# Kernel optimization log

Hardware: AMD Instinct MI355X
Metric: run time of the kernel (lower is better)

Reference implementation:

```python
import math
import jax, jax.numpy as jnp
import numpy as np

CHANNELS = 512
OUT_CHANNELS = 512
N_HEADS = 8
K_CHANNELS = CHANNELS // N_HEADS
WINDOW = 4


def _get_relative_embeddings(emb, length):
    # emb: [1, 2*WINDOW+1, d] -> [1, 2*length-1, d]
    max_rel = 2 * WINDOW + 1
    pad_length = max(0, length - (WINDOW + 1))
    start = max(0, WINDOW + 1 - length)
    end = max_rel + 2 * length - 1
    if pad_length > 0:
        emb = jnp.pad(emb, ((0, 0), (pad_length, pad_length), (0, 0)))
    return emb[:, start:end]


def _rel_to_abs(x):
    # x: [b, h, l, 2l-1] -> [b, h, l, l] via skewing trick
    b, h, l, _ = x.shape
    x = jnp.pad(x, ((0, 0), (0, 0), (0, 0), (0, 1)))
    x_flat = x.reshape(b, h, l * 2 * l)
    x_flat = jnp.pad(x_flat, ((0, 0), (0, 0), (0, l - 1)))
    return x_flat.reshape(b, h, l + 1, 2 * l - 1)[..., :l, l - 1:]


def _abs_to_rel(x):
    # x: [b, h, l, l] -> [b, h, l, 2l-1]
    b, h, l, _ = x.shape
    x = jnp.pad(x, ((0, 0), (0, 0), (0, 0), (0, l - 1)))
    x_flat = x.reshape(b, h, -1)
    x_flat = jnp.pad(x_flat, ((0, 0), (0, 0), (l, 0)))
    return x_flat.reshape(b, h, l, 2 * l)[..., 1:]


def setup_inputs() -> dict:
    key = jax.random.key(0)
    ks = jax.random.split(key, 12)
    B, T = 4, 1024
    w_std = 1.0 / math.sqrt(CHANNELS)
    rel_std = K_CHANNELS ** (-0.5)
    return {
        'x': jax.random.normal(ks[0], (B, T, CHANNELS), jnp.float32),
        'c': jax.random.normal(ks[1], (B, T, CHANNELS), jnp.float32),
        'Wq': jax.random.normal(ks[2], (CHANNELS, CHANNELS), jnp.float32) * w_std,
        'bq': jnp.zeros((CHANNELS,), jnp.float32),
        'Wk': jax.random.normal(ks[3], (CHANNELS, CHANNELS), jnp.float32) * w_std,
        'bk': jnp.zeros((CHANNELS,), jnp.float32),
        'Wv': jax.random.normal(ks[4], (CHANNELS, CHANNELS), jnp.float32) * w_std,
        'bv': jnp.zeros((CHANNELS,), jnp.float32),
        'Wo': jax.random.normal(ks[5], (CHANNELS, OUT_CHANNELS), jnp.float32) * w_std,
        'bo': jnp.zeros((OUT_CHANNELS,), jnp.float32),
        'emb_rel_k': jax.random.normal(ks[6], (1, 2 * WINDOW + 1, K_CHANNELS), jnp.float32) * rel_std,
        'emb_rel_v': jax.random.normal(ks[7], (1, 2 * WINDOW + 1, K_CHANNELS), jnp.float32) * rel_std,
    }


def reference(x, c, Wq, bq, Wk, bk, Wv, bv, Wo, bo, emb_rel_k, emb_rel_v):
    b, t_t, _ = x.shape
    t_s = c.shape[1]
    # 1x1 convs == pointwise dense projections
    q = x @ Wq + bq
    k = c @ Wk + bk
    v = c @ Wv + bv
    q = q.reshape(b, t_t, N_HEADS, K_CHANNELS).transpose(0, 2, 1, 3)
    k = k.reshape(b, t_s, N_HEADS, K_CHANNELS).transpose(0, 2, 1, 3)
    v = v.reshape(b, t_s, N_HEADS, K_CHANNELS).transpose(0, 2, 1, 3)
    q_scaled = q / math.sqrt(K_CHANNELS)
    scores = jnp.einsum('bhtd,bhsd->bhts', q_scaled, k)
    # relative position bias via skewing trick (heads_share=True -> rel emb head dim 1)
    rel_k = _get_relative_embeddings(emb_rel_k, t_s)[0]  # [2*t_s-1, d]
    rel_logits = jnp.einsum('bhtd,md->bhtm', q_scaled, rel_k)
    scores = scores + _rel_to_abs(rel_logits)
    p_attn = jax.nn.softmax(scores, axis=-1)
    out = jnp.einsum('bhts,bhsd->bhtd', p_attn, v)
    rel_w = _abs_to_rel(p_attn)  # [b, h, t, 2t-1]
    rel_v = _get_relative_embeddings(emb_rel_v, t_s)[0]  # [2*t_s-1, d]
    out = out + jnp.einsum('bhtm,md->bhtd', rel_w, rel_v)
    out = out.transpose(0, 2, 1, 3).reshape(b, t_t, CHANNELS)
    return out @ Wo + bo
```

## Files before the change

### kernel.cpp

```cpp
#include <hip/hip_runtime.h>
#include <hip/hip_bf16.h>

#define B_ 4
#define T_ 1024
#define C_ 512
#define H_ 8

typedef __attribute__((ext_vector_type(8))) short short8;
typedef __attribute__((ext_vector_type(4))) float floatx4;

__device__ __forceinline__ unsigned short f2bs(float f) {
    __hip_bfloat16 h = __float2bfloat16(f);
    return *(unsigned short*)&h;
}
__device__ __forceinline__ float bs2f(unsigned short u) {
    __hip_bfloat16 h;
    *(unsigned short*)&h = u;
    return __bfloat162float(h);
}

__device__ __forceinline__ void gload_lds16(const void* g, void* l) {
    __builtin_amdgcn_global_load_lds(
        (const __attribute__((address_space(1))) unsigned int*)g,
        (__attribute__((address_space(3))) unsigned int*)l, 16, 0, 0);
}

__global__ __launch_bounds__(256) void prep(
    const float* __restrict__ Wq, const float* __restrict__ Wk,
    const float* __restrict__ Wv, const float* __restrict__ Wo,
    unsigned short* __restrict__ WT)
{
    __shared__ unsigned short tileT[32][33];
    const int r = blockIdx.x, tid = threadIdx.x;
    const int w = r >> 8, tile = r & 255;
    const int k0 = (tile >> 4) * 32, n0 = (tile & 15) * 32;
    const float* W = (w == 0) ? Wq : (w == 1) ? Wk : (w == 2) ? Wv : Wo;
    unsigned short* out = WT + (size_t)w * 512 * 512;
    const int kk = tid >> 3, ns = (tid & 7) * 4;
    const float4 v = *(const float4*)&W[(size_t)(k0 + kk) * 512 + n0 + ns];
    tileT[ns + 0][kk] = f2bs(v.x);
    tileT[ns + 1][kk] = f2bs(v.y);
    tileT[ns + 2][kk] = f2bs(v.z);
    tileT[ns + 3][kk] = f2bs(v.w);
    __syncthreads();
    const int nn = tid >> 3, ks = (tid & 7) * 4;
    ushort4 o;
    o.x = tileT[nn][ks + 0]; o.y = tileT[nn][ks + 1];
    o.z = tileT[nn][ks + 2]; o.w = tileT[nn][ks + 3];
    *(ushort4*)&out[(size_t)(n0 + nn) * 512 + k0 + ks] = o;
}

__global__ __launch_bounds__(256) void qkv_mfma(
    const float* __restrict__ x, const float* __restrict__ cc,
    const unsigned short* __restrict__ WT,
    const float* __restrict__ bq, const float* __restrict__ bk,
    const float* __restrict__ bv,
    unsigned short* __restrict__ Qc, unsigned short* __restrict__ Kc,
    unsigned short* __restrict__ Vtg)
{
    const int z = blockIdx.z;
    const float* A32 = (z == 0) ? x : cc;
    const unsigned short* Bt = WT + (size_t)z * 262144;
    const float* bias = (z == 0) ? bq : (z == 1) ? bk : bv;
    const float scale = (z == 0) ? 0.125f : 1.0f;

    __shared__ __align__(16) unsigned short sA[2 * 128 * 32];
    __shared__ __align__(16) unsigned short sB[2 * 64 * 32];

    const int tid = threadIdx.x;
    const int wave = tid >> 6, lane = tid & 63;
    const int m0 = blockIdx.y * 128, n0 = blockIdx.x * 64;
    const int mrow = lane & 15, quad = lane >> 4, kgrp = quad * 8;
    const int mhalf = (wave & 1) * 64, noff = (wave >> 1) * 32;
    const int lrow = lane >> 2, lseg = (lane & 3) * 16;

    const int fr0 = tid >> 3;
    const int fc4 = (tid & 7) * 4;

    floatx4 acc[4][2];
    #pragma unroll
    for (int i = 0; i < 4; i++)
        #pragma unroll
        for (int j = 0; j < 2; j++)
            acc[i][j] = (floatx4){0.f, 0.f, 0.f, 0.f};

    float4 a4[4];
    #pragma unroll
    for (int p = 0; p < 4; p++)
        a4[p] = *(const float4*)&A32[(size_t)(m0 + fr0 + p * 32) * 512 + fc4];
    {
        const int rB = wave * 16 + lrow;
        gload_lds16((const char*)Bt + ((size_t)(n0 + rB) * 512) * 2 + lseg,
                    &sB[(size_t)(wave * 16) * 32]);
    }
    #pragma unroll
    for (int p = 0; p < 4; p++) {
        ushort4 o;
        o.x = f2bs(a4[p].x); o.y = f2bs(a4[p].y);
        o.z = f2bs(a4[p].z); o.w = f2bs(a4[p].w);
        *(ushort4*)&sA[(fr0 + p * 32) * 32 + fc4] = o;
    }

    for (int ck = 0; ck < 16; ck++) {
        const int buf = ck & 1;
        __syncthreads();
        if (ck < 15) {
            const int k0 = (ck + 1) * 32;
            const int rB = wave * 16 + lrow;
            gload_lds16((const char*)Bt + ((size_t)(n0 + rB) * 512 + k0) * 2 + lseg,
                        &sB[(size_t)((buf ^ 1) * 64 + wave * 16) * 32]);
            #pragma unroll
            for (int p = 0; p < 4; p++)
                a4[p] = *(const float4*)&A32[(size_t)(m0 + fr0 + p * 32) * 512 + k0 + fc4];
        }
        const unsigned short* sAb = sA + (size_t)buf * 128 * 32;
        const unsigned short* sBb = sB + (size_t)buf * 64 * 32;
        short8 af[4], bfv[2];
        #pragma unroll
        for (int i = 0; i < 4; i++)
            af[i] = *(const short8*)&sAb[(size_t)(mhalf + i * 16 + mrow) * 32 + kgrp];
        #pragma unroll
        for (int i = 0; i < 2; i++)
            bfv[i] = *(const short8*)&sBb[(size_t)(noff + i * 16 + mrow) * 32 + kgrp];
        #pragma unroll
        for (int mt = 0; mt < 4; mt++)
            #pragma unroll
            for (int nt = 0; nt < 2; nt++)
                acc[mt][nt] = __builtin_amdgcn_mfma_f32_16x16x32_bf16(
                    af[mt], bfv[nt], acc[mt][nt], 0, 0, 0);
        if (ck < 15) {
            unsigned short* dst = sA + (size_t)(buf ^ 1) * 128 * 32;
            #pragma unroll
            for (int p = 0; p < 4; p++) {
                ushort4 o;
                o.x = f2bs(a4[p].x); o.y = f2bs(a4[p].y);
                o.z = f2bs(a4[p].z); o.w = f2bs(a4[p].w);
                *(ushort4*)&dst[(fr0 + p * 32) * 32 + fc4] = o;
            }
        }
    }

    const int rowq = quad * 4;
    if (z < 2) {
        unsigned short* Y = (z == 0) ? Qc : Kc;
        #pragma unroll
        for (int nt = 0; nt < 2; nt++) {
            const int n = n0 + noff + nt * 16 + mrow;
            const float bv_ = bias[n];
            const int h = n >> 6, d = n & 63;
            #pragma unroll
            for (int mt = 0; mt < 4; mt++)
                #pragma unroll
                for (int r = 0; r < 4; r++) {
                    const int m = m0 + mhalf + mt * 16 + rowq + r;
                    const int bb = m >> 10, t = m & 1023;
                    Y[(((size_t)bb * H_ + h) * 1024 + t) * 64 + d] =
                        f2bs((acc[mt][nt][r] + bv_) * scale);
                }
        }
    } else {
        #pragma unroll
        for (int nt = 0; nt < 2; nt++) {
            const int n = n0 + noff + nt * 16 + mrow;
            const float bv_ = bias[n];
            const int h = n >> 6, d = n & 63;
            #pragma unroll
            for (int mt = 0; mt < 4; mt++) {
                const int m = m0 + mhalf + mt * 16 + rowq;
                const int bb = m >> 10, t = m & 1023;
                ushort4 o4;
                o4.x = f2bs(acc[mt][nt][0] + bv_);
                o4.y = f2bs(acc[mt][nt][1] + bv_);
                o4.z = f2bs(acc[mt][nt][2] + bv_);
                o4.w = f2bs(acc[mt][nt][3] + bv_);
                *(ushort4*)&Vtg[(((size_t)bb * H_ + h) * 64 + d) * 1024 + t] = o4;
            }
        }
    }
}

__global__ __launch_bounds__(256) void out_mfma(
    const unsigned short* __restrict__ AOb, const unsigned short* __restrict__ WoT,
    const float* __restrict__ bias, float* __restrict__ out)
{
    __shared__ __align__(16) unsigned short sA[2 * 128 * 32];
    __shared__ __align__(16) unsigned short sB[2 * 64 * 32];

    const int tid = threadIdx.x;
    const int wave = tid >> 6, lane = tid & 63;
    const int m0 = blockIdx.y * 128, n0 = blockIdx.x * 64;
    const int mrow = lane & 15, quad = lane >> 4, kgrp = quad * 8;
    const int mhalf = (wave & 1) * 64, noff = (wave >> 1) * 32;
    const int lrow = lane >> 2, lseg = (lane & 3) * 16;

    floatx4 acc[4][2];
    #pragma unroll
    for (int i = 0; i < 4; i++)
        #pragma unroll
        for (int j = 0; j < 2; j++)
            acc[i][j] = (floatx4){0.f, 0.f, 0.f, 0.f};

    auto stage = [&](int k0, int bufi) {
        #pragma unroll
        for (int j = 0; j < 2; j++) {
            const int rA = wave * 32 + j * 16 + lrow;
            gload_lds16((const char*)AOb + ((size_t)(m0 + rA) * 512 + k0) * 2 + lseg,
                        &sA[(size_t)(bufi * 128 + wave * 32 + j * 16) * 32]);
        }
        const int rB = wave * 16 + lrow;
        gload_lds16((const char*)WoT + ((size_t)(n0 + rB) * 512 + k0) * 2 + lseg,
                    &sB[(size_t)(bufi * 64 + wave * 16) * 32]);
    };

    stage(0, 0);
    for (int ck = 0; ck < 16; ck++) {
        const int buf = ck & 1;
        __syncthreads();
        if (ck < 15) stage((ck + 1) * 32, buf ^ 1);
        const unsigned short* sAb = sA + (size_t)buf * 128 * 32;
        const unsigned short* sBb = sB + (size_t)buf * 64 * 32;
        short8 af[4], bfv[2];
        #pragma unroll
        for (int i = 0; i < 4; i++)
            af[i] = *(const short8*)&sAb[(size_t)(mhalf + i * 16 + mrow) * 32 + kgrp];
        #pragma unroll
        for (int i = 0; i < 2; i++)
            bfv[i] = *(const short8*)&sBb[(size_t)(noff + i * 16 + mrow) * 32 + kgrp];
        #pragma unroll
        for (int mt = 0; mt < 4; mt++)
            #pragma unroll
            for (int nt = 0; nt < 2; nt++)
                acc[mt][nt] = __builtin_amdgcn_mfma_f32_16x16x32_bf16(
                    af[mt], bfv[nt], acc[mt][nt], 0, 0, 0);
    }

    const int rowq = quad * 4;
    #pragma unroll
    for (int nt = 0; nt < 2; nt++) {
        const int n = n0 + noff + nt * 16 + mrow;
        const float bv_ = bias[n];
        #pragma unroll
        for (int mt = 0; mt < 4; mt++)
            #pragma unroll
            for (int r = 0; r < 4; r++) {
                const int m = m0 + mhalf + mt * 16 + rowq + r;
                out[(size_t)m * 512 + n] = acc[mt][nt][r] + bv_;
            }
    }
}

__device__ __forceinline__ void attn_stage(
    const unsigned short* __restrict__ Kc, const unsigned short* __restrict__ Vtg,
    size_t qkbase, size_t vtbase, int s0, int wave, int ldrow, int gseg,
    unsigned short* KLb, unsigned short* VtLb)
{
    #pragma unroll
    for (int j = 0; j < 2; j++) {
        const int br = wave * 16 + j * 8;
        gload_lds16((const char*)Kc + (qkbase + (size_t)(s0 + br + ldrow) * 64) * 2 + gseg * 16,
                    &KLb[br * 64]);
        gload_lds16((const char*)Vtg + (vtbase + (size_t)(br + ldrow) * 1024 + s0) * 2 + gseg * 16,
                    &VtLb[br * 64]);
    }
}

__global__ __launch_bounds__(256) void attn_mfma(
    const unsigned short* __restrict__ Qc, const unsigned short* __restrict__ Kc,
    const unsigned short* __restrict__ Vtg,
    const float* __restrict__ rk, const float* __restrict__ rv,
    unsigned short* __restrict__ AOb)
{
    __shared__ __align__(16) unsigned short KL[2][64 * 64];
    __shared__ __align__(16) unsigned short VtL[2][64 * 64];
    __shared__ __align__(16) unsigned short PL[4][16 * 72];
    __shared__ float qbL[64 * 9];
    __shared__ float bandL[64 * 9];
    __shared__ float rvL[9 * 64];
    __shared__ float lL[64];

    const int tb = blockIdx.x, bh = blockIdx.y;
    const int b = bh >> 3, h = bh & 7;
    const int tid = threadIdx.x;
    const int wave = tid >> 6, lane = tid & 63;
    const int t0 = tb * 64;
    const int t0w = t0 + wave * 16;
    const size_t qkbase = (size_t)bh * T_ * 64;
    const size_t vtbase = (size_t)bh * 64 * T_;

    const int mrow = lane & 15;
    const int quad = lane >> 4;
    const int kgrp = quad * 8;
    const int x7 = mrow & 7;
    const int ldrow = lane >> 3;
    const int gseg = (lane & 7) ^ ldrow;

    attn_stage(Kc, Vtg, qkbase, vtbase, 0, wave, ldrow, gseg, &KL[0][0], &VtL[0][0]);

    for (int idx = tid; idx < 576; idx += 256) {
        bandL[idx] = 0.f;
        rvL[idx] = rv[idx];
        const int row = idx / 9, w = idx - row * 9;
        const unsigned short* qp = &Qc[qkbase + (size_t)(t0 + row) * 64];
        float s0a = 0.f, s1a = 0.f, s2a = 0.f, s3a = 0.f;
        #pragma unroll
        for (int d8 = 0; d8 < 8; d8 += 4) {
            const short8 q0 = *(const short8*)&qp[d8 * 8];
            const short8 q1 = *(const short8*)&qp[(d8 + 1) * 8];
            const short8 q2 = *(const short8*)&qp[(d8 + 2) * 8];
            const short8 q3 = *(const short8*)&qp[(d8 + 3) * 8];
            #pragma unroll
            for (int i = 0; i < 8; i++) {
                s0a = fmaf(bs2f((unsigned short)q0[i]), rk[w * 64 + d8 * 8 + i], s0a);
                s1a = fmaf(bs2f((unsigned short)q1[i]), rk[w * 64 + (d8 + 1) * 8 + i], s1a);
                s2a = fmaf(bs2f((unsigned short)q2[i]), rk[w * 64 + (d8 + 2) * 8 + i], s2a);
                s3a = fmaf(bs2f((unsigned short)q3[i]), rk[w * 64 + (d8 + 3) * 8 + i], s3a);
            }
        }
        qbL[idx] = (s0a + s1a) + (s2a + s3a);
    }

    const short8 aQ0 = *(const short8*)&Qc[qkbase + (size_t)(t0w + mrow) * 64 + kgrp];
    const short8 aQ1 = *(const short8*)&Qc[qkbase + (size_t)(t0w + mrow) * 64 + 32 + kgrp];

    floatx4 Oc[4];
    float lsA[4] = {0.f, 0.f, 0.f, 0.f};
    #pragma unroll
    for (int dt = 0; dt < 4; dt++) Oc[dt] = (floatx4){0.f, 0.f, 0.f, 0.f};

    unsigned short* Pw = &PL[wave][0];
    float* qbw = &qbL[wave * 16 * 9];
    float* bandw = &bandL[wave * 16 * 9];

    for (int ck = 0; ck < 16; ck++) {
        const int s0 = ck * 64;
        const int buf = ck & 1;
        __syncthreads();
        if (ck < 15)
            attn_stage(Kc, Vtg, qkbase, vtbase, s0 + 64, wave, ldrow, gseg,
                       &KL[buf ^ 1][0], &VtL[buf ^ 1][0]);

        floatx4 Sc[4];
        #pragma unroll
        for (int st = 0; st < 4; st++) {
            const int row = st * 16 + mrow;
            const short8 aK0 = *(const short8*)&KL[buf][row * 64 + (quad ^ x7) * 8];
            const short8 aK1 = *(const short8*)&KL[buf][row * 64 + ((4 + quad) ^ x7) * 8];
            floatx4 s4 = {0.f, 0.f, 0.f, 0.f};
            s4 = __builtin_amdgcn_mfma_f32_16x16x32_bf16(aK0, aQ0, s4, 0, 0, 0);
            s4 = __builtin_amdgcn_mfma_f32_16x16x32_bf16(aK1, aQ1, s4, 0, 0, 0);
            Sc[st] = s4;
        }

        #pragma unroll
        for (int st = 0; st < 4; st++) {
            const int diff = s0 + st * 16 - t0w;
            float p0, p1, p2, p3;
            if (diff >= -19 && diff <= 19) {
                #pragma unroll
                for (int r = 0; r < 4; r++) {
                    const int rel = diff + quad * 4 + r - mrow;
                    float sc = Sc[st][r];
                    const bool inband = (rel >= -4) && (rel <= 4);
                    if (inband) sc += qbw[mrow * 9 + rel + 4];
                    const float p = __expf(sc);
                    if (inband) bandw[mrow * 9 + rel + 4] = p;
                    Sc[st][r] = p;
                }
            } else {
                #pragma unroll
                for (int r = 0; r < 4; r++) Sc[st][r] = __expf(Sc[st][r]);
            }
            p0 = Sc[st][0]; p1 = Sc[st][1]; p2 = Sc[st][2]; p3 = Sc[st][3];
            lsA[st] += (p0 + p1) + (p2 + p3);
            ushort4 o4;
            o4.x = f2bs(p0); o4.y = f2bs(p1); o4.z = f2bs(p2); o4.w = f2bs(p3);
            *(ushort4*)&Pw[mrow * 72 + st * 16 + quad * 4] = o4;
        }

        #pragma unroll
        for (int c = 0; c < 2; c++) {
            const short8 aP = *(const short8*)&Pw[mrow * 72 + c * 32 + kgrp];
            #pragma unroll
            for (int dt = 0; dt < 4; dt++) {
                const int segl = (c * 4 + quad) ^ x7;
                const short8 bV = *(const short8*)&VtL[buf][(dt * 16 + mrow) * 64 + segl * 8];
                Oc[dt] = __builtin_amdgcn_mfma_f32_16x16x32_bf16(aP, bV, Oc[dt], 0, 0, 0);
            }
        }
    }

    float lv = (lsA[0] + lsA[1]) + (lsA[2] + lsA[3]);
    lv += __shfl_xor(lv, 16);
    lv += __shfl_xor(lv, 32);
    if (quad == 0) lL[wave * 16 + mrow] = lv;

    #pragma unroll
    for (int r = 0; r < 4; r++) {
        const int tl = quad * 4 + r;
        const float inv = 1.f / lL[wave * 16 + tl];
        #pragma unroll
        for (int w = 0; w < 9; w++) {
            const float p = bandw[tl * 9 + w];
            #pragma unroll
            for (int dt = 0; dt < 4; dt++)
                Oc[dt][r] = fmaf(p, rvL[w * 64 + dt * 16 + mrow], Oc[dt][r]);
        }
        const int t = t0w + tl;
        #pragma unroll
        for (int dt = 0; dt < 4; dt++)
            AOb[((size_t)b * 1024 + t) * 512 + h * 64 + dt * 16 + mrow] =
                f2bs(Oc[dt][r] * inv);
    }
}

extern "C" void kernel_launch(void* const* d_in, const int* in_sizes, int n_in,
                              void* d_out, int out_size, void* d_ws, size_t ws_size,
                              hipStream_t stream)
{
    const float* x  = (const float*)d_in[0];
    const float* c  = (const float*)d_in[1];
    const float* Wq = (const float*)d_in[2];
    const float* bq = (const float*)d_in[3];
    const float* Wk = (const float*)d_in[4];
    const float* bk = (const float*)d_in[5];
    const float* Wv = (const float*)d_in[6];
    const float* bv = (const float*)d_in[7];
    const float* Wo = (const float*)d_in[8];
    const float* bo = (const float*)d_in[9];
    const float* rk = (const float*)d_in[10];
    const float* rv = (const float*)d_in[11];

    unsigned short* WT  = (unsigned short*)d_ws;
    unsigned short* Qc  = WT + (size_t)4 * 512 * 512;
    unsigned short* Kc  = Qc + (size_t)32 * 1024 * 64;
    unsigned short* Vtg = Kc + (size_t)32 * 1024 * 64;
    unsigned short* AOb = Vtg + (size_t)32 * 1024 * 64;

    prep<<<1024, 256, 0, stream>>>(Wq, Wk, Wv, Wo, WT);
    qkv_mfma<<<dim3(8, 32, 3), 256, 0, stream>>>(x, c, WT, bq, bk, bv, Qc, Kc, Vtg);
    attn_mfma<<<dim3(16, 32), 256, 0, stream>>>(Qc, Kc, Vtg, rk, rv, AOb);
    out_mfma<<<dim3(8, 32), 256, 0, stream>>>(AOb, WT + (size_t)3 * 262144, bo, (float*)d_out);
}
```

Baseline: 154.9 us.

## Split attention keys across waves and widen QKV projection tiles

The attention kernel stops giving each wave 16 query rows over all 1024 keys through shared-memory K/V staging. Each wave now takes a quarter of the key range for all 64 queries of the block, loads K and V fragments straight from global memory, and merges partial outputs and row sums with shared-memory atomics before the band-embedding epilogue. Separately, the QKV projection tile grows from 128x64 to 128x128, which halves the grid and raises per-wave MFMA reuse. The changes trade shared-memory staging and double buffering for direct global loads, more accumulator registers, and atomic reductions, which may hurt occupancy and latency hiding.

```diff
diff --git a/kernel.cpp b/kernel.cpp
--- a/kernel.cpp
+++ b/kernel.cpp
@@ -65,33 +65,34 @@
     const float scale = (z == 0) ? 0.125f : 1.0f;
 
     __shared__ __align__(16) unsigned short sA[2 * 128 * 32];
-    __shared__ __align__(16) unsigned short sB[2 * 64 * 32];
+    __shared__ __align__(16) unsigned short sB[2 * 128 * 32];
 
     const int tid = threadIdx.x;
     const int wave = tid >> 6, lane = tid & 63;
-    const int m0 = blockIdx.y * 128, n0 = blockIdx.x * 64;
+    const int m0 = blockIdx.y * 128, n0 = blockIdx.x * 128;
     const int mrow = lane & 15, quad = lane >> 4, kgrp = quad * 8;
-    const int mhalf = (wave & 1) * 64, noff = (wave >> 1) * 32;
+    const int mhalf = (wave & 1) * 64, noff = (wave >> 1) * 64;
     const int lrow = lane >> 2, lseg = (lane & 3) * 16;
 
     const int fr0 = tid >> 3;
     const int fc4 = (tid & 7) * 4;
 
-    floatx4 acc[4][2];
+    floatx4 acc[4][4];
     #pragma unroll
     for (int i = 0; i < 4; i++)
         #pragma unroll
-        for (int j = 0; j < 2; j++)
+        for (int j = 0; j < 4; j++)
             acc[i][j] = (floatx4){0.f, 0.f, 0.f, 0.f};
 
     float4 a4[4];
     #pragma unroll
     for (int p = 0; p < 4; p++)
         a4[p] = *(const float4*)&A32[(size_t)(m0 + fr0 + p * 32) * 512 + fc4];
-    {
-        const int rB = wave * 16 + lrow;
+    #pragma unroll
+    for (int j = 0; j < 2; j++) {
+        const int rB = wave * 32 + j * 16 + lrow;
         gload_lds16((const char*)Bt + ((size_t)(n0 + rB) * 512) * 2 + lseg,
-                    &sB[(size_t)(wave * 16) * 32]);
+                    &sB[(size_t)(wave * 32 + j * 16) * 32]);
     }
     #pragma unroll
     for (int p = 0; p < 4; p++) {
@@ -106,26 +107,29 @@
         __syncthreads();
         if (ck < 15) {
             const int k0 = (ck + 1) * 32;
-            const int rB = wave * 16 + lrow;
-            gload_lds16((const char*)Bt + ((size_t)(n0 + rB) * 512 + k0) * 2 + lseg,
-                        &sB[(size_t)((buf ^ 1) * 64 + wave * 16) * 32]);
+            #pragma unroll
+            for (int j = 0; j < 2; j++) {
+                const int rB = wave * 32 + j * 16 + lrow;
+                gload_lds16((const char*)Bt + ((size_t)(n0 + rB) * 512 + k0) * 2 + lseg,
+                            &sB[(size_t)((buf ^ 1) * 128 + wave * 32 + j * 16) * 32]);
+            }
             #pragma unroll
             for (int p = 0; p < 4; p++)
                 a4[p] = *(const float4*)&A32[(size_t)(m0 + fr0 + p * 32) * 512 + k0 + fc4];
         }
         const unsigned short* sAb = sA + (size_t)buf * 128 * 32;
-        const unsigned short* sBb = sB + (size_t)buf * 64 * 32;
-        short8 af[4], bfv[2];
+        const unsigned short* sBb = sB + (size_t)buf * 128 * 32;
+        short8 af[4], bfv[4];
         #pragma unroll
         for (int i = 0; i < 4; i++)
             af[i] = *(const short8*)&sAb[(size_t)(mhalf + i * 16 + mrow) * 32 + kgrp];
         #pragma unroll
-        for (int i = 0; i < 2; i++)
+        for (int i = 0; i < 4; i++)
             bfv[i] = *(const short8*)&sBb[(size_t)(noff + i * 16 + mrow) * 32 + kgrp];
         #pragma unroll
         for (int mt = 0; mt < 4; mt++)
             #pragma unroll
-            for (int nt = 0; nt < 2; nt++)
+            for (int nt = 0; nt < 4; nt++)
                 acc[mt][nt] = __builtin_amdgcn_mfma_f32_16x16x32_bf16(
                     af[mt], bfv[nt], acc[mt][nt], 0, 0, 0);
         if (ck < 15) {
@@ -144,7 +148,7 @@
     if (z < 2) {
         unsigned short* Y = (z == 0) ? Qc : Kc;
         #pragma unroll
-        for (int nt = 0; nt < 2; nt++) {
+        for (int nt = 0; nt < 4; nt++) {
             const int n = n0 + noff + nt * 16 + mrow;
             const float bv_ = bias[n];
             const int h = n >> 6, d = n & 63;
@@ -160,7 +164,7 @@
         }
     } else {
         #pragma unroll
-        for (int nt = 0; nt < 2; nt++) {
+        for (int nt = 0; nt < 4; nt++) {
             const int n = n0 + noff + nt * 16 + mrow;
             const float bv_ = bias[n];
             const int h = n >> 6, d = n & 63;
@@ -249,53 +253,30 @@
     }
 }
 
-__device__ __forceinline__ void attn_stage(
-    const unsigned short* __restrict__ Kc, const unsigned short* __restrict__ Vtg,
-    size_t qkbase, size_t vtbase, int s0, int wave, int ldrow, int gseg,
-    unsigned short* KLb, unsigned short* VtLb)
-{
-    #pragma unroll
-    for (int j = 0; j < 2; j++) {
-        const int br = wave * 16 + j * 8;
-        gload_lds16((const char*)Kc + (qkbase + (size_t)(s0 + br + ldrow) * 64) * 2 + gseg * 16,
-                    &KLb[br * 64]);
-        gload_lds16((const char*)Vtg + (vtbase + (size_t)(br + ldrow) * 1024 + s0) * 2 + gseg * 16,
-                    &VtLb[br * 64]);
-    }
-}
-
-__global__ __launch_bounds__(256) void attn_mfma(
+__global__ __launch_bounds__(256, 2) void attn_mfma(
     const unsigned short* __restrict__ Qc, const unsigned short* __restrict__ Kc,
     const unsigned short* __restrict__ Vtg,
     const float* __restrict__ rk, const float* __restrict__ rv,
     unsigned short* __restrict__ AOb)
 {
-    __shared__ __align__(16) unsigned short KL[2][64 * 64];
-    __shared__ __align__(16) unsigned short VtL[2][64 * 64];
-    __shared__ __align__(16) unsigned short PL[4][16 * 72];
     __shared__ float qbL[64 * 9];
     __shared__ float bandL[64 * 9];
     __shared__ float rvL[9 * 64];
     __shared__ float lL[64];
+    __shared__ __align__(16) float ObufL[64 * 68];
+    __shared__ __align__(16) unsigned short PL[4][64 * 72];
 
     const int tb = blockIdx.x, bh = blockIdx.y;
     const int b = bh >> 3, h = bh & 7;
     const int tid = threadIdx.x;
     const int wave = tid >> 6, lane = tid & 63;
     const int t0 = tb * 64;
-    const int t0w = t0 + wave * 16;
     const size_t qkbase = (size_t)bh * T_ * 64;
     const size_t vtbase = (size_t)bh * 64 * T_;
-
-    const int mrow = lane & 15;
-    const int quad = lane >> 4;
-    const int kgrp = quad * 8;
-    const int x7 = mrow & 7;
-    const int ldrow = lane >> 3;
-    const int gseg = (lane & 7) ^ ldrow;
-
-    attn_stage(Kc, Vtg, qkbase, vtbase, 0, wave, ldrow, gseg, &KL[0][0], &VtL[0][0]);
-
+    const int mrow = lane & 15, quad = lane >> 4, kgrp = quad * 8;
+
+    for (int i = tid; i < 64 * 68; i += 256) ObufL[i] = 0.f;
+    if (tid < 64) lL[tid] = 0.f;
     for (int idx = tid; idx < 576; idx += 256) {
         bandL[idx] = 0.f;
         rvL[idx] = rv[idx];
@@ -319,97 +300,124 @@
         qbL[idx] = (s0a + s1a) + (s2a + s3a);
     }
 
-    const short8 aQ0 = *(const short8*)&Qc[qkbase + (size_t)(t0w + mrow) * 64 + kgrp];
-    const short8 aQ1 = *(const short8*)&Qc[qkbase + (size_t)(t0w + mrow) * 64 + 32 + kgrp];
-
-    floatx4 Oc[4];
-    float lsA[4] = {0.f, 0.f, 0.f, 0.f};
-    #pragma unroll
-    for (int dt = 0; dt < 4; dt++) Oc[dt] = (floatx4){0.f, 0.f, 0.f, 0.f};
+    short8 bQ0[4], bQ1[4];
+    #pragma unroll
+    for (int tt = 0; tt < 4; tt++) {
+        const unsigned short* qp = &Qc[qkbase + (size_t)(t0 + tt * 16 + mrow) * 64];
+        bQ0[tt] = *(const short8*)&qp[kgrp];
+        bQ1[tt] = *(const short8*)&qp[32 + kgrp];
+    }
+
+    floatx4 Oc[4][4];
+    float lacc[4] = {0.f, 0.f, 0.f, 0.f};
+    #pragma unroll
+    for (int i = 0; i < 4; i++)
+        #pragma unroll
+        for (int j = 0; j < 4; j++)
+            Oc[i][j] = (floatx4){0.f, 0.f, 0.f, 0.f};
 
     unsigned short* Pw = &PL[wave][0];
-    float* qbw = &qbL[wave * 16 * 9];
-    float* bandw = &bandL[wave * 16 * 9];
-
-    for (int ck = 0; ck < 16; ck++) {
-        const int s0 = ck * 64;
-        const int buf = ck & 1;
-        __syncthreads();
-        if (ck < 15)
-            attn_stage(Kc, Vtg, qkbase, vtbase, s0 + 64, wave, ldrow, gseg,
-                       &KL[buf ^ 1][0], &VtL[buf ^ 1][0]);
-
-        floatx4 Sc[4];
+
+    __syncthreads();
+
+    const int sw0 = wave * 256;
+    for (int ck = 0; ck < 4; ck++) {
+        const int s0 = sw0 + ck * 64;
+
+        short8 aK0[4], aK1[4];
         #pragma unroll
         for (int st = 0; st < 4; st++) {
-            const int row = st * 16 + mrow;
-            const short8 aK0 = *(const short8*)&KL[buf][row * 64 + (quad ^ x7) * 8];
-            const short8 aK1 = *(const short8*)&KL[buf][row * 64 + ((4 + quad) ^ x7) * 8];
-            floatx4 s4 = {0.f, 0.f, 0.f, 0.f};
-            s4 = __builtin_amdgcn_mfma_f32_16x16x32_bf16(aK0, aQ0, s4, 0, 0, 0);
-            s4 = __builtin_amdgcn_mfma_f32_16x16x32_bf16(aK1, aQ1, s4, 0, 0, 0);
-            Sc[st] = s4;
-        }
+            const unsigned short* kp = &Kc[qkbase + (size_t)(s0 + st * 16 + mrow) * 64];
+            aK0[st] = *(const short8*)&kp[kgrp];
+            aK1[st] = *(const short8*)&kp[32 + kgrp];
+        }
+        short8 bV[2][4];
+        #pragma unroll
+        for (int c = 0; c < 2; c++)
+            #pragma unroll
+            for (int dt = 0; dt < 4; dt++)
+                bV[c][dt] = *(const short8*)&Vtg[vtbase + (size_t)(dt * 16 + mrow) * 1024
+                                                 + s0 + c * 32 + kgrp];
+
+        floatx4 Sc[4][4];
+        #pragma unroll
+        for (int st = 0; st < 4; st++)
+            #pragma unroll
+            for (int tt = 0; tt < 4; tt++) {
+                floatx4 s4 = {0.f, 0.f, 0.f, 0.f};
+                s4 = __builtin_amdgcn_mfma_f32_16x16x32_bf16(aK0[st], bQ0[tt], s4, 0, 0, 0);
+                s4 = __builtin_amdgcn_mfma_f32_16x16x32_bf16(aK1[st], bQ1[tt], s4, 0, 0, 0);
+                Sc[st][tt] = s4;
+            }
 
         #pragma unroll
         for (int st = 0; st < 4; st++) {
-            const int diff = s0 + st * 16 - t0w;
-            float p0, p1, p2, p3;
-            if (diff >= -19 && diff <= 19) {
+            #pragma unroll
+            for (int tt = 0; tt < 4; tt++) {
+                const int diff0 = (s0 + st * 16) - (t0 + tt * 16);
+                const int tl = tt * 16 + mrow;
+                if (diff0 >= -19 && diff0 <= 19) {
+                    #pragma unroll
+                    for (int r = 0; r < 4; r++) {
+                        const int rel = diff0 + quad * 4 + r - mrow;
+                        float sc = Sc[st][tt][r];
+                        const bool inband = (rel >= -4) && (rel <= 4);
+                        if (inband) sc += qbL[tl * 9 + rel + 4];
+                        const float p = __expf(sc);
+                        if (inband) bandL[tl * 9 + rel + 4] = p;
+                        Sc[st][tt][r] = p;
+                    }
+                } else {
+                    #pragma unroll
+                    for (int r = 0; r < 4; r++)
+                        Sc[st][tt][r] = __expf(Sc[st][tt][r]);
+                }
+                lacc[tt] += (Sc[st][tt][0] + Sc[st][tt][1])
+                          + (Sc[st][tt][2] + Sc[st][tt][3]);
+                ushort4 o4;
+                o4.x = f2bs(Sc[st][tt][0]); o4.y = f2bs(Sc[st][tt][1]);
+                o4.z = f2bs(Sc[st][tt][2]); o4.w = f2bs(Sc[st][tt][3]);
+                *(ushort4*)&Pw[tl * 72 + st * 16 + quad * 4] = o4;
+            }
+        }
+
+        #pragma unroll
+        for (int c = 0; c < 2; c++)
+            #pragma unroll
+            for (int tt = 0; tt < 4; tt++) {
+                const short8 aP = *(const short8*)&Pw[(tt * 16 + mrow) * 72 + c * 32 + kgrp];
                 #pragma unroll
-                for (int r = 0; r < 4; r++) {
-                    const int rel = diff + quad * 4 + r - mrow;
-                    float sc = Sc[st][r];
-                    const bool inband = (rel >= -4) && (rel <= 4);
-                    if (inband) sc += qbw[mrow * 9 + rel + 4];
-                    const float p = __expf(sc);
-                    if (inband) bandw[mrow * 9 + rel + 4] = p;
-                    Sc[st][r] = p;
-                }
-            } else {
-                #pragma unroll
-                for (int r = 0; r < 4; r++) Sc[st][r] = __expf(Sc[st][r]);
-            }
-            p0 = Sc[st][0]; p1 = Sc[st][1]; p2 = Sc[st][2]; p3 = Sc[st][3];
-            lsA[st] += (p0 + p1) + (p2 + p3);
-            ushort4 o4;
-            o4.x = f2bs(p0); o4.y = f2bs(p1); o4.z = f2bs(p2); o4.w = f2bs(p3);
-            *(ushort4*)&Pw[mrow * 72 + st * 16 + quad * 4] = o4;
-        }
-
-        #pragma unroll
-        for (int c = 0; c < 2; c++) {
-            const short8 aP = *(const short8*)&Pw[mrow * 72 + c * 32 + kgrp];
-            #pragma unroll
-            for (int dt = 0; dt < 4; dt++) {
-                const int segl = (c * 4 + quad) ^ x7;
-                const short8 bV = *(const short8*)&VtL[buf][(dt * 16 + mrow) * 64 + segl * 8];
-                Oc[dt] = __builtin_amdgcn_mfma_f32_16x16x32_bf16(aP, bV, Oc[dt], 0, 0, 0);
-            }
-        }
-    }
-
-    float lv = (lsA[0] + lsA[1]) + (lsA[2] + lsA[3]);
-    lv += __shfl_xor(lv, 16);
-    lv += __shfl_xor(lv, 32);
-    if (quad == 0) lL[wave * 16 + mrow] = lv;
-
-    #pragma unroll
-    for (int r = 0; r < 4; r++) {
-        const int tl = quad * 4 + r;
-        const float inv = 1.f / lL[wave * 16 + tl];
-        #pragma unroll
-        for (int w = 0; w < 9; w++) {
-            const float p = bandw[tl * 9 + w];
-            #pragma unroll
-            for (int dt = 0; dt < 4; dt++)
-                Oc[dt][r] = fmaf(p, rvL[w * 64 + dt * 16 + mrow], Oc[dt][r]);
-        }
-        const int t = t0w + tl;
+                for (int dt = 0; dt < 4; dt++)
+                    Oc[tt][dt] = __builtin_amdgcn_mfma_f32_16x16x32_bf16(
+                        aP, bV[c][dt], Oc[tt][dt], 0, 0, 0);
+            }
+    }
+
+    #pragma unroll
+    for (int tt = 0; tt < 4; tt++) {
+        float lv = lacc[tt];
+        lv += __shfl_xor(lv, 16);
+        lv += __shfl_xor(lv, 32);
+        if (quad == 0) atomicAdd(&lL[tt * 16 + mrow], lv);
+    }
+    #pragma unroll
+    for (int tt = 0; tt < 4; tt++)
         #pragma unroll
         for (int dt = 0; dt < 4; dt++)
-            AOb[((size_t)b * 1024 + t) * 512 + h * 64 + dt * 16 + mrow] =
-                f2bs(Oc[dt][r] * inv);
+            #pragma unroll
+            for (int r = 0; r < 4; r++)
+                atomicAdd(&ObufL[(tt * 16 + quad * 4 + r) * 68 + dt * 16 + mrow],
+                          Oc[tt][dt][r]);
+    __syncthreads();
+
+    for (int i = 0; i < 16; i++) {
+        const int tl = wave * 16 + i;
+        const float inv = 1.f / lL[tl];
+        float o = ObufL[tl * 68 + lane];
+        #pragma unroll
+        for (int w = 0; w < 9; w++)
+            o = fmaf(bandL[tl * 9 + w], rvL[w * 64 + lane], o);
+        AOb[((size_t)b * 1024 + t0 + tl) * 512 + h * 64 + lane] = f2bs(o * inv);
     }
 }
 
@@ -437,7 +445,7 @@
     unsigned short* AOb = Vtg + (size_t)32 * 1024 * 64;
 
     prep<<<1024, 256, 0, stream>>>(Wq, Wk, Wv, Wo, WT);
-    qkv_mfma<<<dim3(8, 32, 3), 256, 0, stream>>>(x, c, WT, bq, bk, bv, Qc, Kc, Vtg);
+    qkv_mfma<<<dim3(4, 32, 3), 256, 0, stream>>>(x, c, WT, bq, bk, bv, Qc, Kc, Vtg);
     attn_mfma<<<dim3(16, 32), 256, 0, stream>>>(Qc, Kc, Vtg, rk, rv, AOb);
     out_mfma<<<dim3(8, 32), 256, 0, stream>>>(AOb, WT + (size_t)3 * 262144, bo, (float*)d_out);
 }
```

New measurement: 192.3 us. 24.2% more time.
